# Kernel tuning notes

Measured on AMD Instinct MI355X. Metric: run time of the kernel, lower is better.

## Reference

```python
import jax, jax.numpy as jnp
import numpy as np

N_NODES = 10000
NEG_SLOPE = 0.2
EPS = 1e-16


def gat_layer(x, W, a_src, a_dst, bias, src, dst):
    # x: [N, Fin], W: [Fin, Fout], a_src/a_dst: [Fout], bias: [Fout]
    h = x @ W                                  # [N, Fout]
    al_s = h @ a_src                           # [N]
    al_d = h @ a_dst                           # [N]
    e = jax.nn.leaky_relu(al_s[src] + al_d[dst], NEG_SLOPE)   # [E]
    # segment softmax over edges grouped by destination node
    m = jax.ops.segment_max(e, dst, num_segments=N_NODES)     # [N]
    ex = jnp.exp(e - m[dst])
    s = jax.ops.segment_sum(ex, dst, num_segments=N_NODES)    # [N]
    alpha = ex / (s[dst] + EPS)                                # [E]
    out = jax.ops.segment_sum(h[src] * alpha[:, None], dst, num_segments=N_NODES)
    return out + bias


def add_self_loops(edge_index):
    loop = jnp.arange(N_NODES, dtype=edge_index.dtype)
    return jnp.concatenate([edge_index, jnp.stack([loop, loop])], axis=1)


def setup_inputs() -> dict:
    key = jax.random.key(0)
    ks = jax.random.split(key, 12)
    F_in, F_hid, F_out = 256, 256, 256
    x = jax.random.normal(ks[0], (N_NODES, F_in), dtype=jnp.float32)
    pos_edge_index = jax.random.randint(ks[1], (2, 320000), 0, N_NODES)
    edge_index = jax.random.randint(ks[2], (2, 100000), 0, N_NODES)
    sc = lambda f: 1.0 / np.sqrt(f)
    Win_W = jax.random.normal(ks[3], (F_in, F_in), dtype=jnp.float32) * sc(F_in)
    Win_b = jnp.zeros((F_in,), dtype=jnp.float32)
    W1 = jax.random.normal(ks[4], (F_in, F_hid), dtype=jnp.float32) * sc(F_in)
    a1_src = jax.random.normal(ks[5], (F_hid,), dtype=jnp.float32) * sc(F_hid)
    a1_dst = jax.random.normal(ks[6], (F_hid,), dtype=jnp.float32) * sc(F_hid)
    b1 = jnp.zeros((F_hid,), dtype=jnp.float32)
    W2 = jax.random.normal(ks[7], (F_hid, F_out), dtype=jnp.float32) * sc(F_hid)
    a2_src = jax.random.normal(ks[8], (F_out,), dtype=jnp.float32) * sc(F_out)
    a2_dst = jax.random.normal(ks[9], (F_out,), dtype=jnp.float32) * sc(F_out)
    b2 = jnp.zeros((F_out,), dtype=jnp.float32)
    return {
        "x": x, "pos_edge_index": pos_edge_index, "edge_index": edge_index,
        "Win_W": Win_W, "Win_b": Win_b,
        "W1": W1, "a1_src": a1_src, "a1_dst": a1_dst, "b1": b1,
        "W2": W2, "a2_src": a2_src, "a2_dst": a2_dst, "b2": b2,
    }


def reference(x, pos_edge_index, edge_index, Win_W, Win_b,
              W1, a1_src, a1_dst, b1, W2, a2_src, a2_dst, b2):
    ei = add_self_loops(pos_edge_index)
    src, dst = ei[0], ei[1]
    h = x @ Win_W + Win_b                       # input_weighting Linear
    h = gat_layer(h, W1, a1_src, a1_dst, b1, src, dst)
    h = gat_layer(h, W2, a2_src, a2_dst, b2, src, dst)
    logits = jnp.sum(h[edge_index[0]] * h[edge_index[1]], axis=-1)
    return logits
```

## Files before the change

kernel.cpp:

```cpp
#include <hip/hip_runtime.h>
#include <math.h>

#define FDIM 256
#define NEG_SLOPE 0.2f

typedef _Float16 half2v __attribute__((ext_vector_type(2)));
typedef _Float16 half4v __attribute__((ext_vector_type(4)));
typedef _Float16 half8v __attribute__((ext_vector_type(8)));
typedef float f32x4 __attribute__((ext_vector_type(4)));


__global__ void build_phase1(const int* __restrict__ pos_ei,
                             int* __restrict__ cnt,
                             const float* __restrict__ W0, const float* __restrict__ W1,
                             const float* __restrict__ W2,
                             _Float16* __restrict__ Wt_hi, _Float16* __restrict__ Wt_lo,
                             int E_pos, int E_tot, int nbE) {
    int b = blockIdx.x;
    int tid = threadIdx.x;
    if (b < nbE) {
        int e = b * 256 + tid;
        if (e < E_tot) {
            int d = (e < E_pos) ? pos_ei[E_pos + e] : (e - E_pos);
            atomicAdd(&cnt[d], 1);
        }
    } else {
        int idx = b - nbE;
        int n = idx & 255, mat = idx >> 8;
        const float* W = (mat == 0) ? W0 : (mat == 1) ? W1 : W2;
        int k = tid;
        float v = W[k * FDIM + n];
        _Float16 hi = (_Float16)v;
        _Float16 lo = (_Float16)(v - (float)hi);
        size_t o = (size_t)mat * FDIM * FDIM + (size_t)n * FDIM + k;
        Wt_hi[o] = hi;
        Wt_lo[o] = lo;
    }
}


template <int MODE>
__global__ __launch_bounds__(256) void gemm_mfma(
        const float* __restrict__ A32,
        const _Float16* __restrict__ A_hi, const _Float16* __restrict__ A_lo,
        const _Float16* __restrict__ Bt_hi, const _Float16* __restrict__ Bt_lo,
        const float* __restrict__ bias,
        const float* __restrict__ a_src, const float* __restrict__ a_dst,
        float* __restrict__ al_s, float* __restrict__ al_d,
        _Float16* __restrict__ C_hi, _Float16* __restrict__ C_lo,
        int M, int nbGemm, int mblk,
        const int* __restrict__ pos_ei, int* __restrict__ cnt_or_fill,
        int* __restrict__ row_ptr, int* __restrict__ fill_or_srcs,
        int E_pos, int E_tot, int N) {
    __shared__ _Float16 As_hi[64][72];
    __shared__ _Float16 As_lo[64][72];
    __shared__ _Float16 Bs_hi[64][72];
    __shared__ _Float16 Bs_lo[64][72];
    int b = blockIdx.x;
    int tid = threadIdx.x;

    if (b >= nbGemm) {
        if (MODE == 0) {
            int* sums = (int*)&As_hi[0][0];
            const int CH = 40;
            const int* cnt = cnt_or_fill;
            int base = tid * CH;
            int s = 0;
            for (int i = 0; i < CH; ++i) {
                int idx = base + i;
                s += (idx < N) ? cnt[idx] : 0;
            }
            sums[tid] = s;
            __syncthreads();
            for (int off = 1; off < 256; off <<= 1) {
                int v = (tid >= off) ? sums[tid - off] : 0;
                __syncthreads();
                sums[tid] += v;
                __syncthreads();
            }
            int run = (tid == 0) ? 0 : sums[tid - 1];
            for (int i = 0; i < CH; ++i) {
                int idx = base + i;
                if (idx < N) {
                    int v = cnt[idx];
                    row_ptr[idx] = run;
                    fill_or_srcs[idx] = run;
                    run += v;
                }
            }
            if (tid == 255) row_ptr[N] = sums[255];
        } else {
            int e = (b - nbGemm) * 256 + tid;
            if (e < E_tot) {
                int s, d;
                if (e < E_pos) { s = pos_ei[e]; d = pos_ei[E_pos + e]; }
                else           { s = e - E_pos; d = s; }
                int pos = atomicAdd(&cnt_or_fill[d], 1);
                fill_or_srcs[pos] = s;
            }
        }
        return;
    }

    int lane = tid & 63, w = tid >> 6;
    int wm = w >> 1, wn = w & 1;
    int quad = lane >> 4, l16 = lane & 15;
    int bx = b % mblk, by = b / mblk;
    int mBase = bx * 64, nBase = by * 64;
    f32x4 acc[2][2] = {};

    for (int k0 = 0; k0 < FDIM; k0 += 64) {
        __syncthreads();
        if (MODE == 0) {
#pragma unroll
            for (int i = 0; i < 4; ++i) {
                int f = tid + i * 256;
                int m = f >> 4, kc = (f & 15) << 2;
                int row = mBase + m;
                float4 a = make_float4(0.f, 0.f, 0.f, 0.f);
                if (row < M) a = *(const float4*)(A32 + (size_t)row * FDIM + k0 + kc);
                _Float16 hx = (_Float16)a.x, hy = (_Float16)a.y;
                _Float16 hz = (_Float16)a.z, hw = (_Float16)a.w;
                half4v hi = {hx, hy, hz, hw};
                half4v lo = {(_Float16)(a.x - (float)hx), (_Float16)(a.y - (float)hy),
                             (_Float16)(a.z - (float)hz), (_Float16)(a.w - (float)hw)};
                *(half4v*)&As_hi[m][kc] = hi;
                *(half4v*)&As_lo[m][kc] = lo;
            }
        } else {
#pragma unroll
            for (int i = 0; i < 2; ++i) {
                int g = tid + i * 256;
                int m = g >> 3, gk = (g & 7) << 3;
                int row = mBase + m;
                half8v hi, lo;
                if (row < M) {
                    size_t off = (size_t)row * FDIM + k0 + gk;
                    hi = *(const half8v*)(A_hi + off);
                    lo = *(const half8v*)(A_lo + off);
                } else {
                    _Float16 z = (_Float16)0.f;
                    hi = (half8v){z, z, z, z, z, z, z, z};
                    lo = hi;
                }
                *(half8v*)&As_hi[m][gk] = hi;
                *(half8v*)&As_lo[m][gk] = lo;
            }
        }
#pragma unroll
        for (int i = 0; i < 2; ++i) {
            int g = tid + i * 256;
            int n = g >> 3, gk = (g & 7) << 3;
            size_t off = (size_t)(nBase + n) * FDIM + k0 + gk;
            *(half8v*)&Bs_hi[n][gk] = *(const half8v*)(Bt_hi + off);
            *(half8v*)&Bs_lo[n][gk] = *(const half8v*)(Bt_lo + off);
        }
        __syncthreads();
#pragma unroll
        for (int ks = 0; ks < 2; ++ks) {
            int kcol = ks * 32 + quad * 8;
            half8v aHi[2], aLo[2], bHi[2], bLo[2];
#pragma unroll
            for (int mt = 0; mt < 2; ++mt) {
                int r = wm * 32 + mt * 16 + l16;
                aHi[mt] = *(const half8v*)&As_hi[r][kcol];
                aLo[mt] = *(const half8v*)&As_lo[r][kcol];
            }
#pragma unroll
            for (int nt = 0; nt < 2; ++nt) {
                int c = wn * 32 + nt * 16 + l16;
                bHi[nt] = *(const half8v*)&Bs_hi[c][kcol];
                bLo[nt] = *(const half8v*)&Bs_lo[c][kcol];
            }
#pragma unroll
            for (int mt = 0; mt < 2; ++mt)
#pragma unroll
                for (int nt = 0; nt < 2; ++nt) {
                    acc[mt][nt] = __builtin_amdgcn_mfma_f32_16x16x32_f16(
                        aHi[mt], bHi[nt], acc[mt][nt], 0, 0, 0);
                    acc[mt][nt] = __builtin_amdgcn_mfma_f32_16x16x32_f16(
                        aHi[mt], bLo[nt], acc[mt][nt], 0, 0, 0);
                    acc[mt][nt] = __builtin_amdgcn_mfma_f32_16x16x32_f16(
                        aLo[mt], bHi[nt], acc[mt][nt], 0, 0, 0);
                }
        }
    }

    int col0 = nBase + wn * 32 + l16;
    int col1 = col0 + 16;
    if (MODE == 0) {
        float b0 = bias[col0], b1v = bias[col1];
#pragma unroll
        for (int mt = 0; mt < 2; ++mt) {
#pragma unroll
            for (int r = 0; r < 4; ++r) {
                int row = mBase + wm * 32 + mt * 16 + quad * 4 + r;
                if (row >= M) continue;
                float o0 = acc[mt][0][r] + b0;
                float o1 = acc[mt][1][r] + b1v;
                _Float16 h0 = (_Float16)o0, h1 = (_Float16)o1;
                size_t p0 = (size_t)row * FDIM + col0;
                size_t p1 = (size_t)row * FDIM + col1;
                C_hi[p0] = h0;              C_hi[p1] = h1;
                C_lo[p0] = (_Float16)(o0 - (float)h0);
                C_lo[p1] = (_Float16)(o1 - (float)h1);
            }
        }
    } else {
        float as0 = a_src[col0], as1 = a_src[col1];
        float ad0 = a_dst[col0], ad1 = a_dst[col1];
#pragma unroll
        for (int mt = 0; mt < 2; ++mt) {
#pragma unroll
            for (int r = 0; r < 4; ++r) {
                int row = mBase + wm * 32 + mt * 16 + quad * 4 + r;
                if (row < M) {
                    C_hi[(size_t)row * FDIM + col0] = (_Float16)acc[mt][0][r];
                    C_hi[(size_t)row * FDIM + col1] = (_Float16)acc[mt][1][r];
                }
                float ps = acc[mt][0][r] * as0 + acc[mt][1][r] * as1;
                float pd = acc[mt][0][r] * ad0 + acc[mt][1][r] * ad1;
#pragma unroll
                for (int off = 8; off; off >>= 1) {
                    ps += __shfl_xor(ps, off);
                    pd += __shfl_xor(pd, off);
                }
                if (l16 == 0 && row < M) {
                    atomicAdd(&al_s[row], ps);
                    atomicAdd(&al_d[row], pd);
                }
            }
        }
    }
}


__global__ __launch_bounds__(256) void softagg(
        const _Float16* __restrict__ t, const float* __restrict__ al_s,
        const float* __restrict__ al_d, const int* __restrict__ row_ptr,
        const int* __restrict__ srcs, const float* __restrict__ bias,
        _Float16* __restrict__ out_hi, _Float16* __restrict__ out_lo, int N) {
    int wave = threadIdx.x >> 6, lane = threadIdx.x & 63;
    int node = blockIdx.x * 4 + wave;
    if (node >= N) return;
    int beg = row_ptr[node], end = row_ptr[node + 1];
    int deg = end - beg;
    float ad = al_d[node];
    const half4v* tb = (const half4v*)t + lane;
    float4 acc = make_float4(0.f, 0.f, 0.f, 0.f);
    float ssum = 0.f;

    if (deg <= 256) {
        float e[4];
        int sj[4];
#pragma unroll
        for (int c = 0; c < 4; ++c) {
            e[c] = -INFINITY;
            sj[c] = 0;
            int j = beg + c * 64 + lane;
            if (j < end) {
                int s = srcs[j];
                float ee = al_s[s] + ad;
                e[c] = (ee > 0.f) ? ee : NEG_SLOPE * ee;
                sj[c] = s * 64;
            }
        }
        float m = fmaxf(fmaxf(e[0], e[1]), fmaxf(e[2], e[3]));
#pragma unroll
        for (int o = 32; o; o >>= 1) m = fmaxf(m, __shfl_xor(m, o));
        float ex[4];
#pragma unroll
        for (int c = 0; c < 4; ++c) {
            ex[c] = (e[c] == -INFINITY) ? 0.f : __expf(e[c] - m);
            ssum += ex[c];
        }
#pragma unroll
        for (int c = 0; c < 4; ++c) {
            int jc = beg + c * 64;
            if (jc >= end) break;
            int cnt = min(64, end - jc);
            int jj = 0;
            for (; jj + 4 <= cnt; jj += 4) {
                float a0 = __shfl(ex[c], jj + 0), a1 = __shfl(ex[c], jj + 1);
                float a2 = __shfl(ex[c], jj + 2), a3 = __shfl(ex[c], jj + 3);
                int r0 = __shfl(sj[c], jj + 0), r1 = __shfl(sj[c], jj + 1);
                int r2 = __shfl(sj[c], jj + 2), r3 = __shfl(sj[c], jj + 3);
                half4v v0 = tb[r0];
                half4v v1 = tb[r1];
                half4v v2 = tb[r2];
                half4v v3 = tb[r3];
                acc.x = fmaf(a0, (float)v0.x, acc.x); acc.y = fmaf(a0, (float)v0.y, acc.y);
                acc.z = fmaf(a0, (float)v0.z, acc.z); acc.w = fmaf(a0, (float)v0.w, acc.w);
                acc.x = fmaf(a1, (float)v1.x, acc.x); acc.y = fmaf(a1, (float)v1.y, acc.y);
                acc.z = fmaf(a1, (float)v1.z, acc.z); acc.w = fmaf(a1, (float)v1.w, acc.w);
                acc.x = fmaf(a2, (float)v2.x, acc.x); acc.y = fmaf(a2, (float)v2.y, acc.y);
                acc.z = fmaf(a2, (float)v2.z, acc.z); acc.w = fmaf(a2, (float)v2.w, acc.w);
                acc.x = fmaf(a3, (float)v3.x, acc.x); acc.y = fmaf(a3, (float)v3.y, acc.y);
                acc.z = fmaf(a3, (float)v3.z, acc.z); acc.w = fmaf(a3, (float)v3.w, acc.w);
            }
            for (; jj < cnt; ++jj) {
                float a = __shfl(ex[c], jj);
                int r = __shfl(sj[c], jj);
                half4v v = tb[r];
                acc.x = fmaf(a, (float)v.x, acc.x); acc.y = fmaf(a, (float)v.y, acc.y);
                acc.z = fmaf(a, (float)v.z, acc.z); acc.w = fmaf(a, (float)v.w, acc.w);
            }
        }
    } else {
        float m = -INFINITY;
        for (int j = beg + lane; j < end; j += 64) {
            float ee = al_s[srcs[j]] + ad;
            ee = (ee > 0.f) ? ee : NEG_SLOPE * ee;
            m = fmaxf(m, ee);
        }
#pragma unroll
        for (int o = 32; o; o >>= 1) m = fmaxf(m, __shfl_xor(m, o));
        for (int jc = beg; jc < end; jc += 64) {
            int j = jc + lane;
            float ex = 0.f;
            int sr = 0;
            if (j < end) {
                int s = srcs[j];
                float ee = al_s[s] + ad;
                ee = (ee > 0.f) ? ee : NEG_SLOPE * ee;
                ex = __expf(ee - m);
                ssum += ex;
                sr = s * 64;
            }
            int cnt = min(64, end - jc);
            for (int jj = 0; jj < cnt; ++jj) {
                float a = __shfl(ex, jj);
                int r = __shfl(sr, jj);
                half4v v = tb[r];
                acc.x = fmaf(a, (float)v.x, acc.x); acc.y = fmaf(a, (float)v.y, acc.y);
                acc.z = fmaf(a, (float)v.z, acc.z); acc.w = fmaf(a, (float)v.w, acc.w);
            }
        }
    }

#pragma unroll
    for (int o = 32; o; o >>= 1) ssum += __shfl_xor(ssum, o);
    float inv = 1.f / (ssum + 1e-16f);
    float4 bv = ((const float4*)bias)[lane];
    float ox = fmaf(acc.x, inv, bv.x);
    float oy = fmaf(acc.y, inv, bv.y);
    float oz = fmaf(acc.z, inv, bv.z);
    float ow = fmaf(acc.w, inv, bv.w);
    _Float16 hx = (_Float16)ox, hy = (_Float16)oy;
    _Float16 hz = (_Float16)oz, hw = (_Float16)ow;
    half4v hi = {hx, hy, hz, hw};
    *(half4v*)(out_hi + (size_t)node * FDIM + lane * 4) = hi;
    if (out_lo) {
        half4v lo = {(_Float16)(ox - (float)hx), (_Float16)(oy - (float)hy),
                     (_Float16)(oz - (float)hz), (_Float16)(ow - (float)hw)};
        *(half4v*)(out_lo + (size_t)node * FDIM + lane * 4) = lo;
    }
}


__global__ __launch_bounds__(256) void edge_dot(const _Float16* __restrict__ h,
                                                const int* __restrict__ ei,
                                                float* __restrict__ out, int EQ) {
    int w = threadIdx.x >> 6, lane = threadIdx.x & 63;
    int e0 = (blockIdx.x * 4 + w) * 2;
    if (e0 >= EQ) return;
    bool has1 = (e0 + 1) < EQ;
    int u0 = ei[e0], v0 = ei[EQ + e0];
    int u1 = has1 ? ei[e0 + 1] : u0;
    int v1 = has1 ? ei[EQ + e0 + 1] : v0;
    const half4v* hb = (const half4v*)h + lane;
    half4v a0 = hb[(size_t)u0 * 64];
    half4v b0 = hb[(size_t)v0 * 64];
    half4v a1 = hb[(size_t)u1 * 64];
    half4v b1 = hb[(size_t)v1 * 64];
    float s0 = (float)a0.x * (float)b0.x + (float)a0.y * (float)b0.y +
               (float)a0.z * (float)b0.z + (float)a0.w * (float)b0.w;
    float s1 = (float)a1.x * (float)b1.x + (float)a1.y * (float)b1.y +
               (float)a1.z * (float)b1.z + (float)a1.w * (float)b1.w;
#pragma unroll
    for (int o = 32; o; o >>= 1) {
        s0 += __shfl_down(s0, o);
        s1 += __shfl_down(s1, o);
    }
    if (lane == 0) {
        out[e0] = s0;
        if (has1) out[e0 + 1] = s1;
    }
}


extern "C" void kernel_launch(void* const* d_in, const int* in_sizes, int n_in,
                              void* d_out, int out_size, void* d_ws, size_t ws_size,
                              hipStream_t stream) {
    const float* x       = (const float*)d_in[0];
    const int*   pos_ei  = (const int*)d_in[1];
    const int*   q_ei    = (const int*)d_in[2];
    const float* Win_W   = (const float*)d_in[3];
    const float* Win_b   = (const float*)d_in[4];
    const float* W1      = (const float*)d_in[5];
    const float* a1_src  = (const float*)d_in[6];
    const float* a1_dst  = (const float*)d_in[7];
    const float* b1      = (const float*)d_in[8];
    const float* W2      = (const float*)d_in[9];
    const float* a2_src  = (const float*)d_in[10];
    const float* a2_dst  = (const float*)d_in[11];
    const float* b2      = (const float*)d_in[12];
    float* logits = (float*)d_out;

    const int N = in_sizes[0] / FDIM;
    const int E_pos = in_sizes[1] / 2;
    const int EQ = in_sizes[2] / 2;
    const int E_tot = E_pos + N;
    const size_t WMAT = (size_t)FDIM * FDIM;
    const size_t NF = (size_t)N * FDIM;

    _Float16* Wt_hi = (_Float16*)d_ws;
    _Float16* Wt_lo = Wt_hi + 3 * WMAT;
    _Float16* h0_hi = Wt_lo + 3 * WMAT;
    _Float16* h0_lo = h0_hi + NF;
    _Float16* t_h   = h0_lo + NF;
    _Float16* h16   = t_h + NF;
    float* al_s1 = (float*)(h16 + NF);
    float* al_d1 = al_s1 + N;
    float* al_s2 = al_d1 + N;
    float* al_d2 = al_s2 + N;
    int* cnt     = (int*)(al_d2 + N);
    int* row_ptr = cnt + N;
    int* fill    = row_ptr + (N + 1);
    int* srcs    = fill + N;

    hipMemsetAsync(al_s1, 0, (size_t)(4 * N) * sizeof(float) + (size_t)N * sizeof(int), stream);

    int nbE = (E_tot + 255) / 256;
    int mblk = (N + 63) / 64;
    int nbGemm = mblk * (FDIM / 64);
    int nblk4 = (N + 3) / 4;

    build_phase1<<<nbE + 768, 256, 0, stream>>>(pos_ei, cnt, Win_W, W1, W2,
                                                Wt_hi, Wt_lo, E_pos, E_tot, nbE);

    gemm_mfma<0><<<nbGemm + 1, 256, 0, stream>>>(
        x, nullptr, nullptr, Wt_hi, Wt_lo, Win_b,
        nullptr, nullptr, nullptr, nullptr, h0_hi, h0_lo,
        N, nbGemm, mblk,
        pos_ei, cnt, row_ptr, fill, E_pos, E_tot, N);

    gemm_mfma<1><<<nbGemm + nbE, 256, 0, stream>>>(
        nullptr, h0_hi, h0_lo, Wt_hi + WMAT, Wt_lo + WMAT, nullptr,
        a1_src, a1_dst, al_s1, al_d1, t_h, nullptr,
        N, nbGemm, mblk,
        pos_ei, fill, nullptr, srcs, E_pos, E_tot, N);

    softagg<<<nblk4, 256, 0, stream>>>(t_h, al_s1, al_d1, row_ptr, srcs, b1,
                                       h0_hi, h0_lo, N);

    gemm_mfma<1><<<nbGemm, 256, 0, stream>>>(
        nullptr, h0_hi, h0_lo, Wt_hi + 2 * WMAT, Wt_lo + 2 * WMAT, nullptr,
        a2_src, a2_dst, al_s2, al_d2, t_h, nullptr,
        N, nbGemm, mblk,
        nullptr, nullptr, nullptr, nullptr, 0, 0, N);

    softagg<<<nblk4, 256, 0, stream>>>(t_h, al_s2, al_d2, row_ptr, srcs, b2,
                                       h16, nullptr, N);

    edge_dot<<<(EQ + 7) / 8, 256, 0, stream>>>(h16, q_ei, logits, EQ);
}
```

Baseline: 230.7 us.

## Process four nodes per wave in softagg and eight edges per wave in edge_dot

The softmax-aggregation kernel now gives each wave four destination nodes instead of one. When all four have degree of at most 64, their gathers of source rows are interleaved so that up to 16 independent loads are in flight at once, and other cases fall back to a generic per-node loop. edge_dot handles eight query edges per wave, loads the indices as int4 vectors and issues more row gathers at once. The aim is to raise memory-level parallelism and hide gather latency in these latency-bound kernels. The cost is higher register pressure, which may lower occupancy, and fewer waves launched in total.

```diff
diff --git a/kernel.cpp b/kernel.cpp
--- a/kernel.cpp
+++ b/kernel.cpp
@@ -235,125 +235,175 @@
 }
 
 
+__device__ __forceinline__ void agg_node_generic(
+        const _Float16* __restrict__ t, const float* __restrict__ al_s,
+        const int* __restrict__ srcs, int beg, int end, float ad, int lane,
+        float4& acc, float& ssum) {
+    const half4v* tb = (const half4v*)t + lane;
+    float m = -INFINITY;
+    for (int j = beg + lane; j < end; j += 64) {
+        float ee = al_s[srcs[j]] + ad;
+        ee = (ee > 0.f) ? ee : NEG_SLOPE * ee;
+        m = fmaxf(m, ee);
+    }
+#pragma unroll
+    for (int o = 32; o; o >>= 1) m = fmaxf(m, __shfl_xor(m, o));
+    for (int jc = beg; jc < end; jc += 64) {
+        int j = jc + lane;
+        float ex = 0.f;
+        int sr = 0;
+        if (j < end) {
+            int s = srcs[j];
+            float ee = al_s[s] + ad;
+            ee = (ee > 0.f) ? ee : NEG_SLOPE * ee;
+            ex = __expf(ee - m);
+            ssum += ex;
+            sr = s * 64;
+        }
+        int cnt = min(64, end - jc);
+        for (int jj = 0; jj < cnt; ++jj) {
+            float a = __shfl(ex, jj);
+            int r = __shfl(sr, jj);
+            half4v v = tb[r];
+            acc.x = fmaf(a, (float)v.x, acc.x); acc.y = fmaf(a, (float)v.y, acc.y);
+            acc.z = fmaf(a, (float)v.z, acc.z); acc.w = fmaf(a, (float)v.w, acc.w);
+        }
+    }
+}
+
+
 __global__ __launch_bounds__(256) void softagg(
         const _Float16* __restrict__ t, const float* __restrict__ al_s,
         const float* __restrict__ al_d, const int* __restrict__ row_ptr,
         const int* __restrict__ srcs, const float* __restrict__ bias,
         _Float16* __restrict__ out_hi, _Float16* __restrict__ out_lo, int N) {
     int wave = threadIdx.x >> 6, lane = threadIdx.x & 63;
-    int node = blockIdx.x * 4 + wave;
-    if (node >= N) return;
-    int beg = row_ptr[node], end = row_ptr[node + 1];
-    int deg = end - beg;
-    float ad = al_d[node];
+    int node0 = (blockIdx.x * 4 + wave) * 4;
+    if (node0 >= N) return;
+    int nn = min(4, N - node0);
+
+    int rp[5];
+#pragma unroll
+    for (int c = 0; c <= 4; ++c) rp[c] = row_ptr[min(node0 + c, N)];
+    int deg[4];
+    bool fast = (nn == 4);
+#pragma unroll
+    for (int c = 0; c < 4; ++c) {
+        deg[c] = rp[c + 1] - rp[c];
+        if (deg[c] > 64) fast = false;
+    }
+
     const half4v* tb = (const half4v*)t + lane;
-    float4 acc = make_float4(0.f, 0.f, 0.f, 0.f);
-    float ssum = 0.f;
-
-    if (deg <= 256) {
-        float e[4];
+    float4 acc[4];
+    float ssum[4];
+#pragma unroll
+    for (int c = 0; c < 4; ++c) {
+        acc[c] = make_float4(0.f, 0.f, 0.f, 0.f);
+        ssum[c] = 0.f;
+    }
+
+    if (fast) {
+        float ad[4], e[4];
         int sj[4];
 #pragma unroll
+        for (int c = 0; c < 4; ++c) ad[c] = al_d[node0 + c];
+#pragma unroll
         for (int c = 0; c < 4; ++c) {
-            e[c] = -INFINITY;
-            sj[c] = 0;
-            int j = beg + c * 64 + lane;
-            if (j < end) {
+            e[c] = -INFINITY; sj[c] = 0;
+            int j = rp[c] + lane;
+            if (j < rp[c + 1]) {
                 int s = srcs[j];
-                float ee = al_s[s] + ad;
+                float ee = al_s[s] + ad[c];
                 e[c] = (ee > 0.f) ? ee : NEG_SLOPE * ee;
                 sj[c] = s * 64;
             }
         }
-        float m = fmaxf(fmaxf(e[0], e[1]), fmaxf(e[2], e[3]));
-#pragma unroll
-        for (int o = 32; o; o >>= 1) m = fmaxf(m, __shfl_xor(m, o));
+        float m[4];
+#pragma unroll
+        for (int c = 0; c < 4; ++c) m[c] = e[c];
+#pragma unroll
+        for (int o = 32; o; o >>= 1) {
+#pragma unroll
+            for (int c = 0; c < 4; ++c) m[c] = fmaxf(m[c], __shfl_xor(m[c], o));
+        }
         float ex[4];
 #pragma unroll
         for (int c = 0; c < 4; ++c) {
-            ex[c] = (e[c] == -INFINITY) ? 0.f : __expf(e[c] - m);
-            ssum += ex[c];
-        }
+            ex[c] = (e[c] == -INFINITY) ? 0.f : __expf(e[c] - m[c]);
+            ssum[c] += ex[c];
+        }
+
+        int ng[4], ngMax = 0;
 #pragma unroll
         for (int c = 0; c < 4; ++c) {
-            int jc = beg + c * 64;
-            if (jc >= end) break;
-            int cnt = min(64, end - jc);
-            int jj = 0;
-            for (; jj + 4 <= cnt; jj += 4) {
-                float a0 = __shfl(ex[c], jj + 0), a1 = __shfl(ex[c], jj + 1);
-                float a2 = __shfl(ex[c], jj + 2), a3 = __shfl(ex[c], jj + 3);
-                int r0 = __shfl(sj[c], jj + 0), r1 = __shfl(sj[c], jj + 1);
-                int r2 = __shfl(sj[c], jj + 2), r3 = __shfl(sj[c], jj + 3);
-                half4v v0 = tb[r0];
-                half4v v1 = tb[r1];
-                half4v v2 = tb[r2];
-                half4v v3 = tb[r3];
-                acc.x = fmaf(a0, (float)v0.x, acc.x); acc.y = fmaf(a0, (float)v0.y, acc.y);
-                acc.z = fmaf(a0, (float)v0.z, acc.z); acc.w = fmaf(a0, (float)v0.w, acc.w);
-                acc.x = fmaf(a1, (float)v1.x, acc.x); acc.y = fmaf(a1, (float)v1.y, acc.y);
-                acc.z = fmaf(a1, (float)v1.z, acc.z); acc.w = fmaf(a1, (float)v1.w, acc.w);
-                acc.x = fmaf(a2, (float)v2.x, acc.x); acc.y = fmaf(a2, (float)v2.y, acc.y);
-                acc.z = fmaf(a2, (float)v2.z, acc.z); acc.w = fmaf(a2, (float)v2.w, acc.w);
-                acc.x = fmaf(a3, (float)v3.x, acc.x); acc.y = fmaf(a3, (float)v3.y, acc.y);
-                acc.z = fmaf(a3, (float)v3.z, acc.z); acc.w = fmaf(a3, (float)v3.w, acc.w);
-            }
-            for (; jj < cnt; ++jj) {
-                float a = __shfl(ex[c], jj);
-                int r = __shfl(sj[c], jj);
-                half4v v = tb[r];
-                acc.x = fmaf(a, (float)v.x, acc.x); acc.y = fmaf(a, (float)v.y, acc.y);
-                acc.z = fmaf(a, (float)v.z, acc.z); acc.w = fmaf(a, (float)v.w, acc.w);
+            ng[c] = (deg[c] + 3) >> 2;
+            ngMax = max(ngMax, ng[c]);
+        }
+        for (int g = 0; g < ngMax; ++g) {
+            int jj = g * 4;
+            float a[4][4];
+            int r[4][4];
+            half4v v[4][4];
+#pragma unroll
+            for (int c = 0; c < 4; ++c) {
+                if (g < ng[c]) {
+#pragma unroll
+                    for (int q = 0; q < 4; ++q) {
+                        a[c][q] = __shfl(ex[c], jj + q);
+                        r[c][q] = __shfl(sj[c], jj + q);
+                    }
+                }
+            }
+#pragma unroll
+            for (int c = 0; c < 4; ++c) {
+                if (g < ng[c]) {
+#pragma unroll
+                    for (int q = 0; q < 4; ++q) v[c][q] = tb[r[c][q]];
+                }
+            }
+#pragma unroll
+            for (int c = 0; c < 4; ++c) {
+                if (g < ng[c]) {
+#pragma unroll
+                    for (int q = 0; q < 4; ++q) {
+                        acc[c].x = fmaf(a[c][q], (float)v[c][q].x, acc[c].x);
+                        acc[c].y = fmaf(a[c][q], (float)v[c][q].y, acc[c].y);
+                        acc[c].z = fmaf(a[c][q], (float)v[c][q].z, acc[c].z);
+                        acc[c].w = fmaf(a[c][q], (float)v[c][q].w, acc[c].w);
+                    }
+                }
             }
         }
     } else {
-        float m = -INFINITY;
-        for (int j = beg + lane; j < end; j += 64) {
-            float ee = al_s[srcs[j]] + ad;
-            ee = (ee > 0.f) ? ee : NEG_SLOPE * ee;
-            m = fmaxf(m, ee);
-        }
-#pragma unroll
-        for (int o = 32; o; o >>= 1) m = fmaxf(m, __shfl_xor(m, o));
-        for (int jc = beg; jc < end; jc += 64) {
-            int j = jc + lane;
-            float ex = 0.f;
-            int sr = 0;
-            if (j < end) {
-                int s = srcs[j];
-                float ee = al_s[s] + ad;
-                ee = (ee > 0.f) ? ee : NEG_SLOPE * ee;
-                ex = __expf(ee - m);
-                ssum += ex;
-                sr = s * 64;
-            }
-            int cnt = min(64, end - jc);
-            for (int jj = 0; jj < cnt; ++jj) {
-                float a = __shfl(ex, jj);
-                int r = __shfl(sr, jj);
-                half4v v = tb[r];
-                acc.x = fmaf(a, (float)v.x, acc.x); acc.y = fmaf(a, (float)v.y, acc.y);
-                acc.z = fmaf(a, (float)v.z, acc.z); acc.w = fmaf(a, (float)v.w, acc.w);
-            }
-        }
-    }
-
-#pragma unroll
-    for (int o = 32; o; o >>= 1) ssum += __shfl_xor(ssum, o);
-    float inv = 1.f / (ssum + 1e-16f);
+        for (int c = 0; c < nn; ++c) {
+            float ad = al_d[node0 + c];
+            agg_node_generic(t, al_s, srcs, rp[c], rp[c + 1], ad, lane,
+                             acc[c], ssum[c]);
+        }
+    }
+
+#pragma unroll
+    for (int o = 32; o; o >>= 1) {
+#pragma unroll
+        for (int c = 0; c < 4; ++c) ssum[c] += __shfl_xor(ssum[c], o);
+    }
     float4 bv = ((const float4*)bias)[lane];
-    float ox = fmaf(acc.x, inv, bv.x);
-    float oy = fmaf(acc.y, inv, bv.y);
-    float oz = fmaf(acc.z, inv, bv.z);
-    float ow = fmaf(acc.w, inv, bv.w);
-    _Float16 hx = (_Float16)ox, hy = (_Float16)oy;
-    _Float16 hz = (_Float16)oz, hw = (_Float16)ow;
-    half4v hi = {hx, hy, hz, hw};
-    *(half4v*)(out_hi + (size_t)node * FDIM + lane * 4) = hi;
-    if (out_lo) {
-        half4v lo = {(_Float16)(ox - (float)hx), (_Float16)(oy - (float)hy),
-                     (_Float16)(oz - (float)hz), (_Float16)(ow - (float)hw)};
-        *(half4v*)(out_lo + (size_t)node * FDIM + lane * 4) = lo;
+    for (int c = 0; c < nn; ++c) {
+        float inv = 1.f / (ssum[c] + 1e-16f);
+        float ox = fmaf(acc[c].x, inv, bv.x);
+        float oy = fmaf(acc[c].y, inv, bv.y);
+        float oz = fmaf(acc[c].z, inv, bv.z);
+        float ow = fmaf(acc[c].w, inv, bv.w);
+        _Float16 hx = (_Float16)ox, hy = (_Float16)oy;
+        _Float16 hz = (_Float16)oz, hw = (_Float16)ow;
+        half4v hi = {hx, hy, hz, hw};
+        int node = node0 + c;
+        *(half4v*)(out_hi + (size_t)node * FDIM + lane * 4) = hi;
+        if (out_lo) {
+            half4v lo = {(_Float16)(ox - (float)hx), (_Float16)(oy - (float)hy),
+                         (_Float16)(oz - (float)hz), (_Float16)(ow - (float)hw)};
+            *(half4v*)(out_lo + (size_t)node * FDIM + lane * 4) = lo;
+        }
     }
 }
 
@@ -362,29 +412,52 @@
                                                 const int* __restrict__ ei,
                                                 float* __restrict__ out, int EQ) {
     int w = threadIdx.x >> 6, lane = threadIdx.x & 63;
-    int e0 = (blockIdx.x * 4 + w) * 2;
+    int e0 = (blockIdx.x * 4 + w) * 8;
     if (e0 >= EQ) return;
-    bool has1 = (e0 + 1) < EQ;
-    int u0 = ei[e0], v0 = ei[EQ + e0];
-    int u1 = has1 ? ei[e0 + 1] : u0;
-    int v1 = has1 ? ei[EQ + e0 + 1] : v0;
+    int u[8], v[8];
+    if (e0 + 7 < EQ) {
+        int4 uu0 = *(const int4*)(ei + e0);
+        int4 uu1 = *(const int4*)(ei + e0 + 4);
+        int4 vv0 = *(const int4*)(ei + EQ + e0);
+        int4 vv1 = *(const int4*)(ei + EQ + e0 + 4);
+        u[0] = uu0.x; u[1] = uu0.y; u[2] = uu0.z; u[3] = uu0.w;
+        u[4] = uu1.x; u[5] = uu1.y; u[6] = uu1.z; u[7] = uu1.w;
+        v[0] = vv0.x; v[1] = vv0.y; v[2] = vv0.z; v[3] = vv0.w;
+        v[4] = vv1.x; v[5] = vv1.y; v[6] = vv1.z; v[7] = vv1.w;
+    } else {
+#pragma unroll
+        for (int q = 0; q < 8; ++q) {
+            int e = min(e0 + q, EQ - 1);
+            u[q] = ei[e];
+            v[q] = ei[EQ + e];
+        }
+    }
     const half4v* hb = (const half4v*)h + lane;
-    half4v a0 = hb[(size_t)u0 * 64];
-    half4v b0 = hb[(size_t)v0 * 64];
-    half4v a1 = hb[(size_t)u1 * 64];
-    half4v b1 = hb[(size_t)v1 * 64];
-    float s0 = (float)a0.x * (float)b0.x + (float)a0.y * (float)b0.y +
-               (float)a0.z * (float)b0.z + (float)a0.w * (float)b0.w;
-    float s1 = (float)a1.x * (float)b1.x + (float)a1.y * (float)b1.y +
-               (float)a1.z * (float)b1.z + (float)a1.w * (float)b1.w;
+    float s[8];
+#pragma unroll
+    for (int half = 0; half < 2; ++half) {
+        half4v a[4], b[4];
+#pragma unroll
+        for (int q = 0; q < 4; ++q) {
+            a[q] = hb[(size_t)u[half * 4 + q] * 64];
+            b[q] = hb[(size_t)v[half * 4 + q] * 64];
+        }
+#pragma unroll
+        for (int q = 0; q < 4; ++q) {
+            s[half * 4 + q] =
+                (float)a[q].x * (float)b[q].x + (float)a[q].y * (float)b[q].y +
+                (float)a[q].z * (float)b[q].z + (float)a[q].w * (float)b[q].w;
+        }
+    }
 #pragma unroll
     for (int o = 32; o; o >>= 1) {
-        s0 += __shfl_down(s0, o);
-        s1 += __shfl_down(s1, o);
+#pragma unroll
+        for (int q = 0; q < 8; ++q) s[q] += __shfl_down(s[q], o);
     }
     if (lane == 0) {
-        out[e0] = s0;
-        if (has1) out[e0 + 1] = s1;
+#pragma unroll
+        for (int q = 0; q < 8; ++q)
+            if (e0 + q < EQ) out[e0 + q] = s[q];
     }
 }
 
@@ -434,7 +507,7 @@
     int nbE = (E_tot + 255) / 256;
     int mblk = (N + 63) / 64;
     int nbGemm = mblk * (FDIM / 64);
-    int nblk4 = (N + 3) / 4;
+    int nblk16 = (N + 15) / 16;
 
     build_phase1<<<nbE + 768, 256, 0, stream>>>(pos_ei, cnt, Win_W, W1, W2,
                                                 Wt_hi, Wt_lo, E_pos, E_tot, nbE);
@@ -451,8 +524,8 @@
         N, nbGemm, mblk,
         pos_ei, fill, nullptr, srcs, E_pos, E_tot, N);
 
-    softagg<<<nblk4, 256, 0, stream>>>(t_h, al_s1, al_d1, row_ptr, srcs, b1,
-                                       h0_hi, h0_lo, N);
+    softagg<<<nblk16, 256, 0, stream>>>(t_h, al_s1, al_d1, row_ptr, srcs, b1,
+                                        h0_hi, h0_lo, N);
 
     gemm_mfma<1><<<nbGemm, 256, 0, stream>>>(
         nullptr, h0_hi, h0_lo, Wt_hi + 2 * WMAT, Wt_lo + 2 * WMAT, nullptr,
@@ -460,8 +533,8 @@
         N, nbGemm, mblk,
         nullptr, nullptr, nullptr, nullptr, 0, 0, N);
 
-    softagg<<<nblk4, 256, 0, stream>>>(t_h, al_s2, al_d2, row_ptr, srcs, b2,
-                                       h16, nullptr, N);
-
-    edge_dot<<<(EQ + 7) / 8, 256, 0, stream>>>(h16, q_ei, logits, EQ);
+    softagg<<<nblk16, 256, 0, stream>>>(t_h, al_s2, al_d2, row_ptr, srcs, b2,
+                                        h16, nullptr, N);
+
+    edge_dot<<<(EQ + 31) / 32, 256, 0, stream>>>(h16, q_ei, logits, EQ);
 }
```

New measurement: 284.5 us. 23.4% more time.
